# Performance work log

Hardware: AMD Instinct MI355X
Metric: run time of the kernel (lower is better)

Reference implementation:

```python
import jax, jax.numpy as jnp
import numpy as np

TOP_K = 8


def setup_inputs() -> dict:
    key = jax.random.key(0)
    k1, k2 = jax.random.split(key)
    hidden_states = jax.random.normal(k1, (4, 4096, 4096), dtype=jnp.float32)
    weight = jax.random.normal(k2, (64, 4096), dtype=jnp.float32) * 0.02
    return {"hidden_states": hidden_states, "weight": weight}


def reference(hidden_states, weight):
    # Flatten [B, S, H] -> [T, H]; gating math is done in float32 (matches .float()).
    h = hidden_states.shape[-1]
    x = hidden_states.reshape(-1, h).astype(jnp.float32)
    # Router logits: [T, E] = [T, H] @ [H, E]
    logits = jnp.einsum('th,eh->te', x, weight.astype(jnp.float32))
    scores = jax.nn.softmax(logits, axis=-1)
    # Top-k expert selection (greedy router)
    topk_weight, topk_idx = jax.lax.top_k(scores, TOP_K)  # [T, K], [T, K]
    # Normalize top-k probabilities (norm_topk_prob=True)
    denom = jnp.sum(topk_weight, axis=-1, keepdims=True) + 1e-20
    topk_weight = topk_weight / denom
    return topk_weight, topk_idx
```

## Files before the change

kernel.cpp:

```cpp
#include <hip/hip_runtime.h>
#include <math.h>

typedef float  f32x4  __attribute__((ext_vector_type(4)));
typedef int    i32x4  __attribute__((ext_vector_type(4)));

#define H      4096
#define E      64
#define TOPK   8
#define TILE_T 16
#define CK     512
#define MS     8
#define NCH    8

__global__ __launch_bounds__(256)
void prep_w(const float* __restrict__ Wg, signed char* __restrict__ Wb)
{
  int n = blockIdx.x * 256 + threadIdx.x;
  int kgrp = n & 3, m = (n >> 2) & 63, e = n >> 8;
  const float* wp = Wg + e * 4096 + m * 64 + kgrp * 16;
  signed char lb[5][16];
  #pragma unroll
  for (int s = 0; s < 16; ++s) {
    long long v = (long long)rint((double)wp[s] * 2199023255552.0);
    #pragma unroll
    for (int j = 0; j < 4; ++j) {
      signed char b = (signed char)(v & 0xff);
      lb[j][s] = b;
      v = (v - b) >> 8;
    }
    lb[4][s] = (signed char)v;
  }
  int lanei = (kgrp << 4) | (e & 15);
  int eq = e >> 4;
  #pragma unroll
  for (int j = 0; j < 5; ++j) {
    i32x4 d;
    #pragma unroll
    for (int r = 0; r < 4; ++r)
      d[r] = (lb[j][4*r] & 0xFF) | ((lb[j][4*r+1] & 0xFF) << 8)
           | ((lb[j][4*r+2] & 0xFF) << 16) | ((lb[j][4*r+3] & 0xFF) << 24);
    *(i32x4*)(Wb + (((size_t)(m * 4 + eq) * 5 + j) << 10) + lanei * 16) = d;
  }
}

__global__ __launch_bounds__(64)
void comp_w(const float* __restrict__ Wg, double* __restrict__ compT)
{
  int e = blockIdx.x;
  int lane = threadIdx.x;
  double s = 0.0;
  #pragma unroll 4
  for (int i = 0; i < 64; ++i)
    s += rint((double)Wg[e * 4096 + i * 64 + lane] * 2199023255552.0);
  #pragma unroll
  for (int off = 32; off >= 1; off >>= 1)
    s += __shfl_xor(s, off);
  if (lane == 0) compT[e] = 8421504.0 * s;
}

__global__ __launch_bounds__(256, 4)
void moe_gate_i8(const float* __restrict__ X, const signed char* __restrict__ Wb,
                 const double* __restrict__ compT, float* __restrict__ out,
                 int n_tokens)
{
  __shared__ char  As[32768];
  __shared__ double Ls[TILE_T * E];

  const int tid  = threadIdx.x;
  const int lane = tid & 63;
  const int w    = tid >> 6;
  const int t0   = blockIdx.x * TILE_T;
  const int l15  = lane & 15;
  const int kg   = lane >> 4;

  i32x4 z = {0, 0, 0, 0};
  int lab = l15 * 0x01010101;
  i32x4 onev = {0x01010101, 0x01010101, 0x01010101, 0x01010101};
  i32x4 labv = {lab, lab, lab, lab};
  i32x4 pr = __builtin_amdgcn_mfma_i32_16x16x64_i8(labv, onev, z, 0, 0, 0);
  i32x4 pc = __builtin_amdgcn_mfma_i32_16x16x64_i8(onev, labv, z, 0, 0, 0);
  int qrow[4], qcol[4];
  #pragma unroll
  for (int r = 0; r < 4; ++r) { qrow[r] = pr[r] >> 6; qcol[r] = pc[r] >> 6; }

  i32x4 acc3 = z, acc4 = z, acc5 = z, acc6 = z, acc7 = z;

  const int tt = tid >> 4;
  const int ks = tid & 15;
  const float* xp = X + (size_t)(t0 + tt) * H + ks * 32;

  const signed char* bpp = Wb + w * 5120 + lane * 16;

  f32x4 xr[8];
  #pragma unroll
  for (int q = 0; q < 8; ++q) xr[q] = *(const f32x4*)(xp + 4 * q);
  xp += CK;

  for (int c = 0; c < NCH; ++c) {
    #pragma unroll
    for (int hf = 0; hf < 2; ++hf) {
      unsigned w32[16];
      #pragma unroll
      for (int r = 0; r < 4; ++r) {
        f32x4 xv = xr[hf * 4 + r];
        #pragma unroll
        for (int jj = 0; jj < 4; ++jj)
          w32[r*4+jj] = ((unsigned)(int)(xv[jj] * 268435456.0f)) ^ 0x00808080u;
      }
      i32x4 W0, W1, W2, W3;
      #pragma unroll
      for (int r = 0; r < 4; ++r) {
        unsigned u0 = w32[4*r], u1 = w32[4*r+1], u2 = w32[4*r+2], u3 = w32[4*r+3];
        unsigned p01, p23;
        p01 = __builtin_amdgcn_perm(u1, u0, 0x04000400u);
        p23 = __builtin_amdgcn_perm(u3, u2, 0x04000400u);
        W0[r] = (int)__builtin_amdgcn_perm(p23, p01, 0x05040100u);
        p01 = __builtin_amdgcn_perm(u1, u0, 0x05010501u);
        p23 = __builtin_amdgcn_perm(u3, u2, 0x05010501u);
        W1[r] = (int)__builtin_amdgcn_perm(p23, p01, 0x05040100u);
        p01 = __builtin_amdgcn_perm(u1, u0, 0x06020602u);
        p23 = __builtin_amdgcn_perm(u3, u2, 0x06020602u);
        W2[r] = (int)__builtin_amdgcn_perm(p23, p01, 0x05040100u);
        p01 = __builtin_amdgcn_perm(u1, u0, 0x07030703u);
        p23 = __builtin_amdgcn_perm(u3, u2, 0x07030703u);
        W3[r] = (int)__builtin_amdgcn_perm(p23, p01, 0x05040100u);
      }
      const int kgrp = ks * 2 + hf;
      const int swzw = (ks & 7) << 4;
      char* base = As + (kgrp << 10) + (((tt << 4) ^ swzw));
      *(i32x4*)(base + 0x000) = W0;
      *(i32x4*)(base + 0x100) = W1;
      *(i32x4*)(base + 0x200) = W2;
      *(i32x4*)(base + 0x300) = W3;
    }
    __syncthreads();

    if (c < NCH - 1) {
      #pragma unroll
      for (int q = 0; q < 8; ++q) xr[q] = *(const f32x4*)(xp + 4 * q);
      xp += CK;
    }

    #pragma unroll
    for (int m = 0; m < MS; ++m) {
      const int kq   = 4 * m + kg;
      const int swzr = ((kq >> 1) & 7) << 4;
      const char* abase = As + (kq << 10) + (((l15 << 4) ^ swzr));
      i32x4 a0 = *(const i32x4*)(abase + 0x000);
      i32x4 a1 = *(const i32x4*)(abase + 0x100);
      i32x4 a2 = *(const i32x4*)(abase + 0x200);
      i32x4 a3 = *(const i32x4*)(abase + 0x300);
      i32x4 b0 = *(const i32x4*)(bpp);
      i32x4 b1 = *(const i32x4*)(bpp + 1024);
      i32x4 b2 = *(const i32x4*)(bpp + 2048);
      i32x4 b3 = *(const i32x4*)(bpp + 3072);
      i32x4 b4 = *(const i32x4*)(bpp + 4096);
      bpp += 20480;
      acc3 = __builtin_amdgcn_mfma_i32_16x16x64_i8(a0, b3, acc3, 0, 0, 0);
      acc4 = __builtin_amdgcn_mfma_i32_16x16x64_i8(a0, b4, acc4, 0, 0, 0);
      acc5 = __builtin_amdgcn_mfma_i32_16x16x64_i8(a1, b4, acc5, 0, 0, 0);
      acc6 = __builtin_amdgcn_mfma_i32_16x16x64_i8(a2, b4, acc6, 0, 0, 0);
      acc7 = __builtin_amdgcn_mfma_i32_16x16x64_i8(a3, b4, acc7, 0, 0, 0);
      acc3 = __builtin_amdgcn_mfma_i32_16x16x64_i8(a1, b2, acc3, 0, 0, 0);
      acc4 = __builtin_amdgcn_mfma_i32_16x16x64_i8(a1, b3, acc4, 0, 0, 0);
      acc5 = __builtin_amdgcn_mfma_i32_16x16x64_i8(a2, b3, acc5, 0, 0, 0);
      acc6 = __builtin_amdgcn_mfma_i32_16x16x64_i8(a3, b3, acc6, 0, 0, 0);
      acc3 = __builtin_amdgcn_mfma_i32_16x16x64_i8(a2, b1, acc3, 0, 0, 0);
      acc4 = __builtin_amdgcn_mfma_i32_16x16x64_i8(a2, b2, acc4, 0, 0, 0);
      acc5 = __builtin_amdgcn_mfma_i32_16x16x64_i8(a3, b2, acc5, 0, 0, 0);
      acc3 = __builtin_amdgcn_mfma_i32_16x16x64_i8(a3, b0, acc3, 0, 0, 0);
      acc4 = __builtin_amdgcn_mfma_i32_16x16x64_i8(a3, b1, acc4, 0, 0, 0);
    }
    __syncthreads();
  }

  #pragma unroll
  for (int r = 0; r < 4; ++r) {
    int ex = w * 16 + qcol[r];
    double part = (16777216.0              * (double)acc3[r]
                 + 4294967296.0            * (double)acc4[r]
                 + 1099511627776.0         * (double)acc5[r]
                 + 281474976710656.0       * (double)acc6[r]
                 + 72057594037927936.0     * (double)acc7[r]
                 + compT[ex]) * 1.6940658945086007e-21;
    Ls[qrow[r] * E + ex] = part;
  }
  __syncthreads();

  for (int tt2 = 0; tt2 < 4; tt2++) {
    int t = w * 4 + tt2;
    double val = Ls[t * E + lane];

    double mx = val;
    #pragma unroll
    for (int off = 32; off >= 1; off >>= 1)
      mx = fmax(mx, __shfl_xor(mx, off));

    float p = expf((float)(val - mx));
    float S = p;
    #pragma unroll
    for (int off = 32; off >= 1; off >>= 1)
      S += __shfl_xor(S, off);

    double cur = val;
    float myw = 0.f; int myidx = 0;
    float psum = 0.f;
    #pragma unroll
    for (int r = 0; r < TOPK; r++) {
      double v = cur; int ii = lane;
      #pragma unroll
      for (int off = 32; off >= 1; off >>= 1) {
        double ov = __shfl_xor(v, off);
        int    oi = __shfl_xor(ii, off);
        if (ov > v || (ov == v && oi < ii)) { v = ov; ii = oi; }
      }
      float pw = __shfl(p, ii);
      psum += pw;
      if (lane == r) { myw = pw; myidx = ii; }
      if (lane == ii) cur = -INFINITY;
    }
    float denom = psum + 1e-20f * S;
    if (lane < TOPK) {
      size_t gt = (size_t)(t0 + t);
      out[gt * TOPK + lane] = myw / denom;
      out[(size_t)n_tokens * TOPK + gt * TOPK + lane] = (float)myidx;
    }
  }
}

extern "C" void kernel_launch(void* const* d_in, const int* in_sizes, int n_in,
                              void* d_out, int out_size, void* d_ws, size_t ws_size,
                              hipStream_t stream)
{
  const float* X  = (const float*)d_in[0];
  const float* Wg = (const float*)d_in[1];
  float* out = (float*)d_out;
  signed char* Wb = (signed char*)d_ws;
  double* compT   = (double*)((char*)d_ws + 1310720);
  int n_tokens = in_sizes[0] / H;

  prep_w<<<64, 256, 0, stream>>>(Wg, Wb);
  comp_w<<<64, 64, 0, stream>>>(Wg, compT);
  moe_gate_i8<<<n_tokens / TILE_T, 256, 0, stream>>>(X, Wb, compT, out, n_tokens);
}
```

Measured before the change: 132.7 us.

## Double token tile to 32 so each weight fragment feeds two MFMA sets

Raises the per-block token tile from 16 to 32 and halves the K chunk, so each loaded B (weight) fragment is reused across two 16-token A fragments with two accumulator sets. This halves the weight-fragment global traffic per token and halves the grid size. It also drops the register prefetch of the next X chunk (loads now happen at the top of each iteration), aliases Ls onto the shared staging buffer, and removes the occupancy hint from launch bounds. The costs are more accumulator registers, possibly lower occupancy, and less overlap of X loads with compute.

```diff
diff --git a/kernel.cpp b/kernel.cpp
--- a/kernel.cpp
+++ b/kernel.cpp
@@ -7,10 +7,10 @@
 #define H      4096
 #define E      64
 #define TOPK   8
-#define TILE_T 16
-#define CK     512
-#define MS     8
-#define NCH    8
+#define TILE_T 32
+#define CK     256
+#define MS     4
+#define NCH    16
 
 __global__ __launch_bounds__(256)
 void prep_w(const float* __restrict__ Wg, signed char* __restrict__ Wb)
@@ -58,13 +58,13 @@
   if (lane == 0) compT[e] = 8421504.0 * s;
 }
 
-__global__ __launch_bounds__(256, 4)
+__global__ __launch_bounds__(256)
 void moe_gate_i8(const float* __restrict__ X, const signed char* __restrict__ Wb,
                  const double* __restrict__ compT, float* __restrict__ out,
                  int n_tokens)
 {
-  __shared__ char  As[32768];
-  __shared__ double Ls[TILE_T * E];
+  __shared__ char sm[32768];
+  double* Ls = (double*)sm;
 
   const int tid  = threadIdx.x;
   const int lane = tid & 63;
@@ -83,20 +83,21 @@
   #pragma unroll
   for (int r = 0; r < 4; ++r) { qrow[r] = pr[r] >> 6; qcol[r] = pc[r] >> 6; }
 
-  i32x4 acc3 = z, acc4 = z, acc5 = z, acc6 = z, acc7 = z;
-
-  const int tt = tid >> 4;
-  const int ks = tid & 15;
+  i32x4 aA3 = z, aA4 = z, aA5 = z, aA6 = z, aA7 = z;
+  i32x4 aB3 = z, aB4 = z, aB5 = z, aB6 = z, aB7 = z;
+
+  const int tt = tid >> 3;
+  const int ks = tid & 7;
   const float* xp = X + (size_t)(t0 + tt) * H + ks * 32;
 
   const signed char* bpp = Wb + w * 5120 + lane * 16;
 
-  f32x4 xr[8];
-  #pragma unroll
-  for (int q = 0; q < 8; ++q) xr[q] = *(const f32x4*)(xp + 4 * q);
-  xp += CK;
-
   for (int c = 0; c < NCH; ++c) {
+    f32x4 xr[8];
+    #pragma unroll
+    for (int q = 0; q < 8; ++q) xr[q] = *(const f32x4*)(xp + 4 * q);
+    xp += CK;
+
     #pragma unroll
     for (int hf = 0; hf < 2; ++hf) {
       unsigned w32[16];
@@ -126,50 +127,62 @@
         W3[r] = (int)__builtin_amdgcn_perm(p23, p01, 0x05040100u);
       }
       const int kgrp = ks * 2 + hf;
-      const int swzw = (ks & 7) << 4;
-      char* base = As + (kgrp << 10) + (((tt << 4) ^ swzw));
+      const int swzw = ks << 4;
+      char* base = sm + (kgrp << 11) + (((tt << 4) ^ swzw));
       *(i32x4*)(base + 0x000) = W0;
-      *(i32x4*)(base + 0x100) = W1;
-      *(i32x4*)(base + 0x200) = W2;
-      *(i32x4*)(base + 0x300) = W3;
+      *(i32x4*)(base + 0x200) = W1;
+      *(i32x4*)(base + 0x400) = W2;
+      *(i32x4*)(base + 0x600) = W3;
     }
     __syncthreads();
-
-    if (c < NCH - 1) {
-      #pragma unroll
-      for (int q = 0; q < 8; ++q) xr[q] = *(const f32x4*)(xp + 4 * q);
-      xp += CK;
-    }
 
     #pragma unroll
     for (int m = 0; m < MS; ++m) {
       const int kq   = 4 * m + kg;
       const int swzr = ((kq >> 1) & 7) << 4;
-      const char* abase = As + (kq << 10) + (((l15 << 4) ^ swzr));
-      i32x4 a0 = *(const i32x4*)(abase + 0x000);
-      i32x4 a1 = *(const i32x4*)(abase + 0x100);
-      i32x4 a2 = *(const i32x4*)(abase + 0x200);
-      i32x4 a3 = *(const i32x4*)(abase + 0x300);
+      const char* abase = sm + (kq << 11) + (((l15 << 4) ^ swzr));
       i32x4 b0 = *(const i32x4*)(bpp);
       i32x4 b1 = *(const i32x4*)(bpp + 1024);
       i32x4 b2 = *(const i32x4*)(bpp + 2048);
       i32x4 b3 = *(const i32x4*)(bpp + 3072);
       i32x4 b4 = *(const i32x4*)(bpp + 4096);
       bpp += 20480;
-      acc3 = __builtin_amdgcn_mfma_i32_16x16x64_i8(a0, b3, acc3, 0, 0, 0);
-      acc4 = __builtin_amdgcn_mfma_i32_16x16x64_i8(a0, b4, acc4, 0, 0, 0);
-      acc5 = __builtin_amdgcn_mfma_i32_16x16x64_i8(a1, b4, acc5, 0, 0, 0);
-      acc6 = __builtin_amdgcn_mfma_i32_16x16x64_i8(a2, b4, acc6, 0, 0, 0);
-      acc7 = __builtin_amdgcn_mfma_i32_16x16x64_i8(a3, b4, acc7, 0, 0, 0);
-      acc3 = __builtin_amdgcn_mfma_i32_16x16x64_i8(a1, b2, acc3, 0, 0, 0);
-      acc4 = __builtin_amdgcn_mfma_i32_16x16x64_i8(a1, b3, acc4, 0, 0, 0);
-      acc5 = __builtin_amdgcn_mfma_i32_16x16x64_i8(a2, b3, acc5, 0, 0, 0);
-      acc6 = __builtin_amdgcn_mfma_i32_16x16x64_i8(a3, b3, acc6, 0, 0, 0);
-      acc3 = __builtin_amdgcn_mfma_i32_16x16x64_i8(a2, b1, acc3, 0, 0, 0);
-      acc4 = __builtin_amdgcn_mfma_i32_16x16x64_i8(a2, b2, acc4, 0, 0, 0);
-      acc5 = __builtin_amdgcn_mfma_i32_16x16x64_i8(a3, b2, acc5, 0, 0, 0);
-      acc3 = __builtin_amdgcn_mfma_i32_16x16x64_i8(a3, b0, acc3, 0, 0, 0);
-      acc4 = __builtin_amdgcn_mfma_i32_16x16x64_i8(a3, b1, acc4, 0, 0, 0);
+      i32x4 xA0 = *(const i32x4*)(abase + 0x000);
+      i32x4 xA1 = *(const i32x4*)(abase + 0x200);
+      i32x4 xA2 = *(const i32x4*)(abase + 0x400);
+      i32x4 xA3 = *(const i32x4*)(abase + 0x600);
+      i32x4 xB0 = *(const i32x4*)(abase + 0x100);
+      i32x4 xB1 = *(const i32x4*)(abase + 0x300);
+      i32x4 xB2 = *(const i32x4*)(abase + 0x500);
+      i32x4 xB3 = *(const i32x4*)(abase + 0x700);
+      aA3 = __builtin_amdgcn_mfma_i32_16x16x64_i8(xA0, b3, aA3, 0, 0, 0);
+      aB3 = __builtin_amdgcn_mfma_i32_16x16x64_i8(xB0, b3, aB3, 0, 0, 0);
+      aA4 = __builtin_amdgcn_mfma_i32_16x16x64_i8(xA0, b4, aA4, 0, 0, 0);
+      aB4 = __builtin_amdgcn_mfma_i32_16x16x64_i8(xB0, b4, aB4, 0, 0, 0);
+      aA5 = __builtin_amdgcn_mfma_i32_16x16x64_i8(xA1, b4, aA5, 0, 0, 0);
+      aB5 = __builtin_amdgcn_mfma_i32_16x16x64_i8(xB1, b4, aB5, 0, 0, 0);
+      aA6 = __builtin_amdgcn_mfma_i32_16x16x64_i8(xA2, b4, aA6, 0, 0, 0);
+      aB6 = __builtin_amdgcn_mfma_i32_16x16x64_i8(xB2, b4, aB6, 0, 0, 0);
+      aA7 = __builtin_amdgcn_mfma_i32_16x16x64_i8(xA3, b4, aA7, 0, 0, 0);
+      aB7 = __builtin_amdgcn_mfma_i32_16x16x64_i8(xB3, b4, aB7, 0, 0, 0);
+      aA3 = __builtin_amdgcn_mfma_i32_16x16x64_i8(xA1, b2, aA3, 0, 0, 0);
+      aB3 = __builtin_amdgcn_mfma_i32_16x16x64_i8(xB1, b2, aB3, 0, 0, 0);
+      aA4 = __builtin_amdgcn_mfma_i32_16x16x64_i8(xA1, b3, aA4, 0, 0, 0);
+      aB4 = __builtin_amdgcn_mfma_i32_16x16x64_i8(xB1, b3, aB4, 0, 0, 0);
+      aA5 = __builtin_amdgcn_mfma_i32_16x16x64_i8(xA2, b3, aA5, 0, 0, 0);
+      aB5 = __builtin_amdgcn_mfma_i32_16x16x64_i8(xB2, b3, aB5, 0, 0, 0);
+      aA6 = __builtin_amdgcn_mfma_i32_16x16x64_i8(xA3, b3, aA6, 0, 0, 0);
+      aB6 = __builtin_amdgcn_mfma_i32_16x16x64_i8(xB3, b3, aB6, 0, 0, 0);
+      aA3 = __builtin_amdgcn_mfma_i32_16x16x64_i8(xA2, b1, aA3, 0, 0, 0);
+      aB3 = __builtin_amdgcn_mfma_i32_16x16x64_i8(xB2, b1, aB3, 0, 0, 0);
+      aA4 = __builtin_amdgcn_mfma_i32_16x16x64_i8(xA2, b2, aA4, 0, 0, 0);
+      aB4 = __builtin_amdgcn_mfma_i32_16x16x64_i8(xB2, b2, aB4, 0, 0, 0);
+      aA5 = __builtin_amdgcn_mfma_i32_16x16x64_i8(xA3, b2, aA5, 0, 0, 0);
+      aB5 = __builtin_amdgcn_mfma_i32_16x16x64_i8(xB3, b2, aB5, 0, 0, 0);
+      aA3 = __builtin_amdgcn_mfma_i32_16x16x64_i8(xA3, b0, aA3, 0, 0, 0);
+      aB3 = __builtin_amdgcn_mfma_i32_16x16x64_i8(xB3, b0, aB3, 0, 0, 0);
+      aA4 = __builtin_amdgcn_mfma_i32_16x16x64_i8(xA3, b1, aA4, 0, 0, 0);
+      aB4 = __builtin_amdgcn_mfma_i32_16x16x64_i8(xB3, b1, aB4, 0, 0, 0);
     }
     __syncthreads();
   }
@@ -177,18 +190,25 @@
   #pragma unroll
   for (int r = 0; r < 4; ++r) {
     int ex = w * 16 + qcol[r];
-    double part = (16777216.0              * (double)acc3[r]
-                 + 4294967296.0            * (double)acc4[r]
-                 + 1099511627776.0         * (double)acc5[r]
-                 + 281474976710656.0       * (double)acc6[r]
-                 + 72057594037927936.0     * (double)acc7[r]
-                 + compT[ex]) * 1.6940658945086007e-21;
-    Ls[qrow[r] * E + ex] = part;
+    double pA = (16777216.0          * (double)aA3[r]
+               + 4294967296.0        * (double)aA4[r]
+               + 1099511627776.0     * (double)aA5[r]
+               + 281474976710656.0   * (double)aA6[r]
+               + 72057594037927936.0 * (double)aA7[r]
+               + compT[ex]) * 1.6940658945086007e-21;
+    double pB = (16777216.0          * (double)aB3[r]
+               + 4294967296.0        * (double)aB4[r]
+               + 1099511627776.0     * (double)aB5[r]
+               + 281474976710656.0   * (double)aB6[r]
+               + 72057594037927936.0 * (double)aB7[r]
+               + compT[ex]) * 1.6940658945086007e-21;
+    Ls[qrow[r] * E + ex]        = pA;
+    Ls[(16 + qrow[r]) * E + ex] = pB;
   }
   __syncthreads();
 
-  for (int tt2 = 0; tt2 < 4; tt2++) {
-    int t = w * 4 + tt2;
+  for (int tt2 = 0; tt2 < 8; tt2++) {
+    int t = w * 8 + tt2;
     double val = Ls[t * E + lane];
 
     double mx = val;
```

Result: slower. 141.3 us (+6.5%).

## Split K dimension four ways with atomic fp64 accumulation and separate top-k kernel

Applied to the files above, without the earlier changes.

Splits the H reduction into four quarters so each block handles one token tile and one K-quarter, quadrupling the grid. Partial fp64 logits are accumulated into a zeroed global buffer with atomics, and a separate kernel then does softmax and top-k. The aim is more parallelism and less per-block serial work. In exchange it drops the register prefetch of X, adds two extra launches, and adds atomic global traffic; fp64 atomic order could perturb exact top-k ties.

```diff
diff --git a/kernel.cpp b/kernel.cpp
--- a/kernel.cpp
+++ b/kernel.cpp
@@ -3,14 +3,20 @@
 
 typedef float  f32x4  __attribute__((ext_vector_type(4)));
 typedef int    i32x4  __attribute__((ext_vector_type(4)));
+typedef double f64x4  __attribute__((ext_vector_type(4)));
 
 #define H      4096
 #define E      64
 #define TOPK   8
 #define TILE_T 16
-#define CK     512
-#define MS     8
-#define NCH    8
+#define KQSZ   1024
+#define CK     256
+#define MS     4
+#define NCH    4
+
+#define WB_OFF   0
+#define COMP_OFF 1310720
+#define LG_OFF   2097152
 
 __global__ __launch_bounds__(256)
 void prep_w(const float* __restrict__ Wg, signed char* __restrict__ Wb)
@@ -46,30 +52,41 @@
 __global__ __launch_bounds__(64)
 void comp_w(const float* __restrict__ Wg, double* __restrict__ compT)
 {
-  int e = blockIdx.x;
+  int b = blockIdx.x;
+  int kQ = b >> 6, e = b & 63;
   int lane = threadIdx.x;
   double s = 0.0;
   #pragma unroll 4
-  for (int i = 0; i < 64; ++i)
-    s += rint((double)Wg[e * 4096 + i * 64 + lane] * 2199023255552.0);
+  for (int i = 0; i < 16; ++i)
+    s += rint((double)Wg[e * 4096 + kQ * 1024 + i * 64 + lane] * 2199023255552.0);
   #pragma unroll
   for (int off = 32; off >= 1; off >>= 1)
     s += __shfl_xor(s, off);
-  if (lane == 0) compT[e] = 8421504.0 * s;
-}
-
-__global__ __launch_bounds__(256, 4)
-void moe_gate_i8(const float* __restrict__ X, const signed char* __restrict__ Wb,
-                 const double* __restrict__ compT, float* __restrict__ out,
-                 int n_tokens)
-{
-  __shared__ char  As[32768];
-  __shared__ double Ls[TILE_T * E];
+  if (lane == 0) compT[kQ * 64 + e] = 8421504.0 * s;
+}
+
+__global__ __launch_bounds__(256)
+void zero_lg(double* __restrict__ lg)
+{
+  size_t i = ((size_t)blockIdx.x * 256 + threadIdx.x) * 4;
+  f64x4 z4 = {0.0, 0.0, 0.0, 0.0};
+  *(f64x4*)(lg + i) = z4;
+}
+
+__global__ __launch_bounds__(256)
+void moe_part(const float* __restrict__ X, const signed char* __restrict__ Wb,
+              const double* __restrict__ compT, double* __restrict__ lg)
+{
+  __shared__ char As[16384];
+
+  const int bid  = blockIdx.x;
+  const int tile = bid >> 2;
+  const int kQ   = bid & 3;
+  const int t0   = tile * TILE_T;
 
   const int tid  = threadIdx.x;
   const int lane = tid & 63;
   const int w    = tid >> 6;
-  const int t0   = blockIdx.x * TILE_T;
   const int l15  = lane & 15;
   const int kg   = lane >> 4;
 
@@ -87,59 +104,51 @@
 
   const int tt = tid >> 4;
   const int ks = tid & 15;
-  const float* xp = X + (size_t)(t0 + tt) * H + ks * 32;
-
-  const signed char* bpp = Wb + w * 5120 + lane * 16;
-
-  f32x4 xr[8];
-  #pragma unroll
-  for (int q = 0; q < 8; ++q) xr[q] = *(const f32x4*)(xp + 4 * q);
-  xp += CK;
+  const float* xp = X + (size_t)(t0 + tt) * H + kQ * KQSZ + ks * 16;
+
+  const signed char* bpp = Wb + (size_t)(kQ * 64 + w) * 5120 + lane * 16;
 
   for (int c = 0; c < NCH; ++c) {
-    #pragma unroll
-    for (int hf = 0; hf < 2; ++hf) {
-      unsigned w32[16];
+    f32x4 xr[4];
+    #pragma unroll
+    for (int q = 0; q < 4; ++q)
+      xr[q] = *(const f32x4*)(xp + c * CK + 4 * q);
+
+    unsigned w32[16];
+    #pragma unroll
+    for (int r = 0; r < 4; ++r) {
+      f32x4 xv = xr[r];
       #pragma unroll
-      for (int r = 0; r < 4; ++r) {
-        f32x4 xv = xr[hf * 4 + r];
-        #pragma unroll
-        for (int jj = 0; jj < 4; ++jj)
-          w32[r*4+jj] = ((unsigned)(int)(xv[jj] * 268435456.0f)) ^ 0x00808080u;
-      }
-      i32x4 W0, W1, W2, W3;
-      #pragma unroll
-      for (int r = 0; r < 4; ++r) {
-        unsigned u0 = w32[4*r], u1 = w32[4*r+1], u2 = w32[4*r+2], u3 = w32[4*r+3];
-        unsigned p01, p23;
-        p01 = __builtin_amdgcn_perm(u1, u0, 0x04000400u);
-        p23 = __builtin_amdgcn_perm(u3, u2, 0x04000400u);
-        W0[r] = (int)__builtin_amdgcn_perm(p23, p01, 0x05040100u);
-        p01 = __builtin_amdgcn_perm(u1, u0, 0x05010501u);
-        p23 = __builtin_amdgcn_perm(u3, u2, 0x05010501u);
-        W1[r] = (int)__builtin_amdgcn_perm(p23, p01, 0x05040100u);
-        p01 = __builtin_amdgcn_perm(u1, u0, 0x06020602u);
-        p23 = __builtin_amdgcn_perm(u3, u2, 0x06020602u);
-        W2[r] = (int)__builtin_amdgcn_perm(p23, p01, 0x05040100u);
-        p01 = __builtin_amdgcn_perm(u1, u0, 0x07030703u);
-        p23 = __builtin_amdgcn_perm(u3, u2, 0x07030703u);
-        W3[r] = (int)__builtin_amdgcn_perm(p23, p01, 0x05040100u);
-      }
-      const int kgrp = ks * 2 + hf;
-      const int swzw = (ks & 7) << 4;
-      char* base = As + (kgrp << 10) + (((tt << 4) ^ swzw));
+      for (int jj = 0; jj < 4; ++jj)
+        w32[r*4+jj] = ((unsigned)(int)(xv[jj] * 268435456.0f)) ^ 0x00808080u;
+    }
+    i32x4 W0, W1, W2, W3;
+    #pragma unroll
+    for (int r = 0; r < 4; ++r) {
+      unsigned u0 = w32[4*r], u1 = w32[4*r+1], u2 = w32[4*r+2], u3 = w32[4*r+3];
+      unsigned p01, p23;
+      p01 = __builtin_amdgcn_perm(u1, u0, 0x04000400u);
+      p23 = __builtin_amdgcn_perm(u3, u2, 0x04000400u);
+      W0[r] = (int)__builtin_amdgcn_perm(p23, p01, 0x05040100u);
+      p01 = __builtin_amdgcn_perm(u1, u0, 0x05010501u);
+      p23 = __builtin_amdgcn_perm(u3, u2, 0x05010501u);
+      W1[r] = (int)__builtin_amdgcn_perm(p23, p01, 0x05040100u);
+      p01 = __builtin_amdgcn_perm(u1, u0, 0x06020602u);
+      p23 = __builtin_amdgcn_perm(u3, u2, 0x06020602u);
+      W2[r] = (int)__builtin_amdgcn_perm(p23, p01, 0x05040100u);
+      p01 = __builtin_amdgcn_perm(u1, u0, 0x07030703u);
+      p23 = __builtin_amdgcn_perm(u3, u2, 0x07030703u);
+      W3[r] = (int)__builtin_amdgcn_perm(p23, p01, 0x05040100u);
+    }
+    {
+      const int swzw = ((ks >> 1) & 7) << 4;
+      char* base = As + (ks << 10) + (((tt << 4) ^ swzw));
       *(i32x4*)(base + 0x000) = W0;
       *(i32x4*)(base + 0x100) = W1;
       *(i32x4*)(base + 0x200) = W2;
       *(i32x4*)(base + 0x300) = W3;
     }
     __syncthreads();
-
-    if (c < NCH - 1) {
-      #pragma unroll
-      for (int q = 0; q < 8; ++q) xr[q] = *(const f32x4*)(xp + 4 * q);
-      xp += CK;
-    }
 
     #pragma unroll
     for (int m = 0; m < MS; ++m) {
@@ -182,14 +191,22 @@
                  + 1099511627776.0         * (double)acc5[r]
                  + 281474976710656.0       * (double)acc6[r]
                  + 72057594037927936.0     * (double)acc7[r]
-                 + compT[ex]) * 1.6940658945086007e-21;
-    Ls[qrow[r] * E + ex] = part;
-  }
-  __syncthreads();
-
-  for (int tt2 = 0; tt2 < 4; tt2++) {
-    int t = w * 4 + tt2;
-    double val = Ls[t * E + lane];
+                 + compT[kQ * 64 + ex]) * 1.6940658945086007e-21;
+    unsafeAtomicAdd(&lg[(size_t)(t0 + qrow[r]) * E + ex], part);
+  }
+}
+
+__global__ __launch_bounds__(256)
+void moe_fin(const double* __restrict__ lg, float* __restrict__ out,
+             int n_tokens)
+{
+  const int tid  = threadIdx.x;
+  const int lane = tid & 63;
+  const int wv   = tid >> 6;
+
+  for (int i = 0; i < 16; ++i) {
+    int t = blockIdx.x * 64 + wv * 16 + i;
+    double val = lg[(size_t)t * E + lane];
 
     double mx = val;
     #pragma unroll
@@ -221,7 +238,7 @@
     }
     float denom = psum + 1e-20f * S;
     if (lane < TOPK) {
-      size_t gt = (size_t)(t0 + t);
+      size_t gt = (size_t)t;
       out[gt * TOPK + lane] = myw / denom;
       out[(size_t)n_tokens * TOPK + gt * TOPK + lane] = (float)myidx;
     }
@@ -235,11 +252,14 @@
   const float* X  = (const float*)d_in[0];
   const float* Wg = (const float*)d_in[1];
   float* out = (float*)d_out;
-  signed char* Wb = (signed char*)d_ws;
-  double* compT   = (double*)((char*)d_ws + 1310720);
+  signed char* Wb = (signed char*)((char*)d_ws + WB_OFF);
+  double* compT   = (double*)((char*)d_ws + COMP_OFF);
+  double* lg      = (double*)((char*)d_ws + LG_OFF);
   int n_tokens = in_sizes[0] / H;
 
   prep_w<<<64, 256, 0, stream>>>(Wg, Wb);
-  comp_w<<<64, 64, 0, stream>>>(Wg, compT);
-  moe_gate_i8<<<n_tokens / TILE_T, 256, 0, stream>>>(X, Wb, compT, out, n_tokens);
-}
+  comp_w<<<256, 64, 0, stream>>>(Wg, compT);
+  zero_lg<<<1024, 256, 0, stream>>>(lg);
+  moe_part<<<(n_tokens / TILE_T) * 4, 256, 0, stream>>>(X, Wb, compT, lg);
+  moe_fin<<<n_tokens / 64, 256, 0, stream>>>(lg, out, n_tokens);
+}
```

Result: slower. 192.9 us (+45.3%).

## Halve K-chunk, coalesce X loads per warp, and alias logits into A tile LDS

Applied to the files above, without the earlier changes.

Shrinks the per-iteration K chunk from 512 to 256 (16 chunks instead of 8) and changes the X load mapping so each warp reads four full token rows with lanes covering contiguous float4s, writing 4-byte words into the swizzled LDS tile. It drops the register prefetch of the next chunk and removes the occupancy hint from launch bounds. The logits buffer now aliases the A tile, cutting LDS to 16KB to allow more resident blocks. The cost is losing software prefetch overlap, doubling barrier count, and using narrower LDS stores.

```diff
diff --git a/kernel.cpp b/kernel.cpp
--- a/kernel.cpp
+++ b/kernel.cpp
@@ -8,9 +8,9 @@
 #define E      64
 #define TOPK   8
 #define TILE_T 16
-#define CK     512
-#define MS     8
-#define NCH    8
+#define CK     256
+#define MS     4
+#define NCH    16
 
 __global__ __launch_bounds__(256)
 void prep_w(const float* __restrict__ Wg, signed char* __restrict__ Wb)
@@ -58,13 +58,13 @@
   if (lane == 0) compT[e] = 8421504.0 * s;
 }
 
-__global__ __launch_bounds__(256, 4)
+__global__ __launch_bounds__(256)
 void moe_gate_i8(const float* __restrict__ X, const signed char* __restrict__ Wb,
                  const double* __restrict__ compT, float* __restrict__ out,
                  int n_tokens)
 {
-  __shared__ char  As[32768];
-  __shared__ double Ls[TILE_T * E];
+  __shared__ char As[16384];
+  double* Ls = (double*)As;
 
   const int tid  = threadIdx.x;
   const int lane = tid & 63;
@@ -85,61 +85,46 @@
 
   i32x4 acc3 = z, acc4 = z, acc5 = z, acc6 = z, acc7 = z;
 
-  const int tt = tid >> 4;
-  const int ks = tid & 15;
-  const float* xp = X + (size_t)(t0 + tt) * H + ks * 32;
+  const int kgrp = lane >> 2;
+  const int wrd  = lane & 3;
+  const int swzs = ((lane >> 3) & 7) << 4;
+  const float* xbase = X + (size_t)t0 * H + lane * 4;
 
   const signed char* bpp = Wb + w * 5120 + lane * 16;
 
-  f32x4 xr[8];
-  #pragma unroll
-  for (int q = 0; q < 8; ++q) xr[q] = *(const f32x4*)(xp + 4 * q);
-  xp += CK;
-
   for (int c = 0; c < NCH; ++c) {
-    #pragma unroll
-    for (int hf = 0; hf < 2; ++hf) {
-      unsigned w32[16];
-      #pragma unroll
-      for (int r = 0; r < 4; ++r) {
-        f32x4 xv = xr[hf * 4 + r];
-        #pragma unroll
-        for (int jj = 0; jj < 4; ++jj)
-          w32[r*4+jj] = ((unsigned)(int)(xv[jj] * 268435456.0f)) ^ 0x00808080u;
-      }
-      i32x4 W0, W1, W2, W3;
-      #pragma unroll
-      for (int r = 0; r < 4; ++r) {
-        unsigned u0 = w32[4*r], u1 = w32[4*r+1], u2 = w32[4*r+2], u3 = w32[4*r+3];
-        unsigned p01, p23;
-        p01 = __builtin_amdgcn_perm(u1, u0, 0x04000400u);
-        p23 = __builtin_amdgcn_perm(u3, u2, 0x04000400u);
-        W0[r] = (int)__builtin_amdgcn_perm(p23, p01, 0x05040100u);
-        p01 = __builtin_amdgcn_perm(u1, u0, 0x05010501u);
-        p23 = __builtin_amdgcn_perm(u3, u2, 0x05010501u);
-        W1[r] = (int)__builtin_amdgcn_perm(p23, p01, 0x05040100u);
-        p01 = __builtin_amdgcn_perm(u1, u0, 0x06020602u);
-        p23 = __builtin_amdgcn_perm(u3, u2, 0x06020602u);
-        W2[r] = (int)__builtin_amdgcn_perm(p23, p01, 0x05040100u);
-        p01 = __builtin_amdgcn_perm(u1, u0, 0x07030703u);
-        p23 = __builtin_amdgcn_perm(u3, u2, 0x07030703u);
-        W3[r] = (int)__builtin_amdgcn_perm(p23, p01, 0x05040100u);
-      }
-      const int kgrp = ks * 2 + hf;
-      const int swzw = (ks & 7) << 4;
-      char* base = As + (kgrp << 10) + (((tt << 4) ^ swzw));
-      *(i32x4*)(base + 0x000) = W0;
-      *(i32x4*)(base + 0x100) = W1;
-      *(i32x4*)(base + 0x200) = W2;
-      *(i32x4*)(base + 0x300) = W3;
+    f32x4 xr[4];
+    #pragma unroll
+    for (int q = 0; q < 4; ++q)
+      xr[q] = *(const f32x4*)(xbase + (size_t)(w * 4 + q) * H + c * CK);
+
+    #pragma unroll
+    for (int q = 0; q < 4; ++q) {
+      const int r = w * 4 + q;
+      unsigned u0 = ((unsigned)(int)(xr[q][0] * 268435456.0f)) ^ 0x00808080u;
+      unsigned u1 = ((unsigned)(int)(xr[q][1] * 268435456.0f)) ^ 0x00808080u;
+      unsigned u2 = ((unsigned)(int)(xr[q][2] * 268435456.0f)) ^ 0x00808080u;
+      unsigned u3 = ((unsigned)(int)(xr[q][3] * 268435456.0f)) ^ 0x00808080u;
+      unsigned p01, p23, W0, W1, W2, W3;
+      p01 = __builtin_amdgcn_perm(u1, u0, 0x04000400u);
+      p23 = __builtin_amdgcn_perm(u3, u2, 0x04000400u);
+      W0  = __builtin_amdgcn_perm(p23, p01, 0x05040100u);
+      p01 = __builtin_amdgcn_perm(u1, u0, 0x05010501u);
+      p23 = __builtin_amdgcn_perm(u3, u2, 0x05010501u);
+      W1  = __builtin_amdgcn_perm(p23, p01, 0x05040100u);
+      p01 = __builtin_amdgcn_perm(u1, u0, 0x06020602u);
+      p23 = __builtin_amdgcn_perm(u3, u2, 0x06020602u);
+      W2  = __builtin_amdgcn_perm(p23, p01, 0x05040100u);
+      p01 = __builtin_amdgcn_perm(u1, u0, 0x07030703u);
+      p23 = __builtin_amdgcn_perm(u3, u2, 0x07030703u);
+      W3  = __builtin_amdgcn_perm(p23, p01, 0x05040100u);
+      char* base = As + (kgrp << 10) + (((r << 4) ^ swzs)) + (wrd << 2);
+      *(unsigned*)(base + 0x000) = W0;
+      *(unsigned*)(base + 0x100) = W1;
+      *(unsigned*)(base + 0x200) = W2;
+      *(unsigned*)(base + 0x300) = W3;
     }
     __syncthreads();
-
-    if (c < NCH - 1) {
-      #pragma unroll
-      for (int q = 0; q < 8; ++q) xr[q] = *(const f32x4*)(xp + 4 * q);
-      xp += CK;
-    }
 
     #pragma unroll
     for (int m = 0; m < MS; ++m) {
```

After: 118.8 us. 1.12x faster.
